# Optimization experiments

Hardware: AMD Instinct MI355X
Metric: run time of the kernel (lower is better)

The kernel has to match this reference:

```python
import jax, jax.numpy as jnp
import numpy as np

NEG_SLOPE = 0.2  # PyG GATConv default LeakyReLU slope
EPS = 1e-16


def gat_layer(x, W, a_src, a_dst, bias, src, dst, heads, out_dim, concat):
    N = x.shape[0]
    h = (x @ W).reshape(N, heads, out_dim)          # [N,H,C]
    alpha_src = (h * a_src).sum(-1)                  # [N,H]
    alpha_dst = (h * a_dst).sum(-1)                  # [N,H]
    e = jax.nn.leaky_relu(alpha_src[src] + alpha_dst[dst], NEG_SLOPE)  # [E,H]
    # segment softmax over incoming edges of each destination node
    m = jax.ops.segment_max(e, dst, num_segments=N)  # [N,H]
    p = jnp.exp(e - m[dst])
    denom = jax.ops.segment_sum(p, dst, num_segments=N)
    alpha = p / (denom[dst] + EPS)                   # [E,H]
    # scatter-aggregate messages to destinations
    out = jax.ops.segment_sum(alpha[:, :, None] * h[src], dst, num_segments=N)  # [N,H,C]
    out = out.reshape(N, heads * out_dim) if concat else out.mean(axis=1)
    return out + bias


def setup_inputs() -> dict:
    N, E, F_IN, NC = 100000, 1600000, 512, 10
    key = jax.random.key(0)
    ks = jax.random.split(key, 9)
    return {
        "x": jax.random.normal(ks[0], (N, F_IN), jnp.float32),
        "W1": jax.random.normal(ks[1], (F_IN, 64), jnp.float32) * (1.0 / np.sqrt(F_IN)),
        "att_src1": jax.random.normal(ks[2], (1, 8, 8), jnp.float32) * 0.1,
        "att_dst1": jax.random.normal(ks[3], (1, 8, 8), jnp.float32) * 0.1,
        "b1": jnp.zeros((64,), jnp.float32),
        "W2": jax.random.normal(ks[4], (64, NC), jnp.float32) * (1.0 / 8.0),
        "att_src2": jax.random.normal(ks[5], (1, 1, NC), jnp.float32) * 0.1,
        "att_dst2": jax.random.normal(ks[6], (1, 1, NC), jnp.float32) * 0.1,
        "b2": jnp.zeros((NC,), jnp.float32),
        "edge_index": jax.random.randint(ks[7], (2, E), 0, N, jnp.int64),
    }


def reference(x, W1, att_src1, att_dst1, b1, W2, att_src2, att_dst2, b2, edge_index):
    N = x.shape[0]
    # add self-loops (PyG GATConv add_self_loops=True default)
    loop = jnp.arange(N, dtype=edge_index.dtype)
    src = jnp.concatenate([edge_index[0], loop])
    dst = jnp.concatenate([edge_index[1], loop])
    h = gat_layer(x, W1, att_src1, att_dst1, b1, src, dst, heads=8, out_dim=8, concat=True)
    h = jax.nn.elu(h)
    nc = W2.shape[1]
    out = gat_layer(h, W2, att_src2, att_dst2, b2, src, dst, heads=1, out_dim=nc, concat=False)
    return jax.nn.log_softmax(out, axis=1)
```

## Files before the change

### kernel.cpp

```cpp
#include <hip/hip_runtime.h>
#include <math.h>

#define NEG 0.2f

typedef __bf16 bf16x4 __attribute__((ext_vector_type(4)));
typedef __bf16 bf16x8 __attribute__((ext_vector_type(8)));
typedef float  f32x4  __attribute__((ext_vector_type(4)));

__global__ __launch_bounds__(256) void gemm1_k(const float* __restrict__ x,
                                               const float* __restrict__ W1,
                                               float* __restrict__ h1, int Nn)
{
    __shared__ __bf16 xs[2][64][40];
    int t = threadIdx.x;
    int wave = t >> 6, lane = t & 63;
    int row0 = blockIdx.x * 64;
    int col0 = wave * 16;
    int lm = lane & 15;
    int lk = lane >> 4;

    bf16x8 bfrag[16];
#pragma unroll
    for (int ch = 0; ch < 16; ++ch) {
        int kb = ch * 32 + lk * 8;
#pragma unroll
        for (int j = 0; j < 8; ++j)
            bfrag[ch][j] = (__bf16)W1[(size_t)(kb + j) * 64 + col0 + lm];
    }

    f32x4 acc[4] = {};

    {
        int r = t >> 3, c4 = t & 7;
#pragma unroll
        for (int p = 0; p < 2; ++p) {
            int rr = p * 32 + r;
            int gr = row0 + rr;
            float4 v = make_float4(0.f, 0.f, 0.f, 0.f);
            if (gr < Nn) v = *(const float4*)(x + (size_t)gr * 512 + c4 * 4);
            bf16x4 b;
            b[0] = (__bf16)v.x; b[1] = (__bf16)v.y; b[2] = (__bf16)v.z; b[3] = (__bf16)v.w;
            *(bf16x4*)&xs[0][rr][c4 * 4] = b;
        }
    }
    __syncthreads();

#pragma unroll
    for (int ch = 0; ch < 16; ++ch) {
        int buf = ch & 1;
        if (ch < 15) {
            int kb = (ch + 1) * 32;
            int r = t >> 3, c4 = t & 7;
#pragma unroll
            for (int p = 0; p < 2; ++p) {
                int rr = p * 32 + r;
                int gr = row0 + rr;
                float4 v = make_float4(0.f, 0.f, 0.f, 0.f);
                if (gr < Nn) v = *(const float4*)(x + (size_t)gr * 512 + kb + c4 * 4);
                bf16x4 b;
                b[0] = (__bf16)v.x; b[1] = (__bf16)v.y; b[2] = (__bf16)v.z; b[3] = (__bf16)v.w;
                *(bf16x4*)&xs[1 - buf][rr][c4 * 4] = b;
            }
        }
#pragma unroll
        for (int rt = 0; rt < 4; ++rt) {
            bf16x8 a = *(bf16x8*)&xs[buf][rt * 16 + lm][lk * 8];
            acc[rt] = __builtin_amdgcn_mfma_f32_16x16x32_bf16(a, bfrag[ch], acc[rt], 0, 0, 0);
        }
        __syncthreads();
    }

#pragma unroll
    for (int rt = 0; rt < 4; ++rt) {
#pragma unroll
        for (int j = 0; j < 4; ++j) {
            int gr = row0 + rt * 16 + lk * 4 + j;
            if (gr < Nn) h1[(size_t)gr * 64 + col0 + lm] = acc[rt][j];
        }
    }
}

__global__ void attn1_k(const float* __restrict__ h1, const float* __restrict__ asrc,
                        const float* __restrict__ adst, float* __restrict__ as1,
                        float* __restrict__ ad1, int Nn)
{
    int tid = blockIdx.x * 256 + threadIdx.x;
    if (tid >= Nn * 8) return;
    int n = tid >> 3, h = tid & 7;
    const float* hp = h1 + (size_t)n * 64 + h * 8;
    float s = 0.f, d = 0.f;
#pragma unroll
    for (int c = 0; c < 8; ++c) {
        float v = hp[c];
        s += v * asrc[h * 8 + c];
        d += v * adst[h * 8 + c];
    }
    as1[tid] = s;
    ad1[tid] = d;
}

__global__ void hist_rank_k(const int* __restrict__ ei, int E, int Nn,
                            int* __restrict__ deg, int* __restrict__ rank)
{
    int e = blockIdx.x * 256 + threadIdx.x;
    int Ep = E + Nn;
    if (e >= Ep) return;
    int d = (e < E) ? ei[E + e] : e - E;
    rank[e] = atomicAdd(&deg[d], 1);
}

__global__ void scan_a_k(const int* __restrict__ deg, int Nn, int* __restrict__ bsum)
{
    __shared__ int tmp[256];
    int t = threadIdx.x;
    int base = blockIdx.x * 1024 + t * 4;
    int s = 0;
#pragma unroll
    for (int j = 0; j < 4; ++j) { int i = base + j; if (i < Nn) s += deg[i]; }
    tmp[t] = s;
    __syncthreads();
    for (int off = 1; off < 256; off <<= 1) {
        int a = (t >= off) ? tmp[t - off] : 0;
        __syncthreads();
        tmp[t] += a;
        __syncthreads();
    }
    if (t == 255) bsum[blockIdx.x] = tmp[255];
}

__global__ void scan_b_k(int* __restrict__ bsum, int nb)
{
    __shared__ int tmp[256];
    int t = threadIdx.x;
    int v = (t < nb) ? bsum[t] : 0;
    tmp[t] = v;
    __syncthreads();
    for (int off = 1; off < 256; off <<= 1) {
        int a = (t >= off) ? tmp[t - off] : 0;
        __syncthreads();
        tmp[t] += a;
        __syncthreads();
    }
    if (t < nb) bsum[t] = tmp[t] - v;
}

__global__ void scan_c_k(const int* __restrict__ deg, int Nn, const int* __restrict__ boff,
                         int* __restrict__ rowptr)
{
    __shared__ int tmp[256];
    int t = threadIdx.x;
    int base = blockIdx.x * 1024 + t * 4;
    int v[4];
    int s = 0;
#pragma unroll
    for (int j = 0; j < 4; ++j) {
        int i = base + j;
        v[j] = (i < Nn) ? deg[i] : 0;
        s += v[j];
    }
    tmp[t] = s;
    __syncthreads();
    for (int off = 1; off < 256; off <<= 1) {
        int a = (t >= off) ? tmp[t - off] : 0;
        __syncthreads();
        tmp[t] += a;
        __syncthreads();
    }
    int excl = boff[blockIdx.x] + tmp[t] - s;
#pragma unroll
    for (int j = 0; j < 4; ++j) {
        int i = base + j;
        if (i < Nn) {
            rowptr[i] = excl;
            excl += v[j];
            if (i == Nn - 1) rowptr[Nn] = excl;
        }
    }
}

__global__ void scat2_k(const int* __restrict__ ei, int E, int Nn,
                        const int* __restrict__ rowptr, const int* __restrict__ rank,
                        int* __restrict__ csr)
{
    int e = blockIdx.x * 256 + threadIdx.x;
    int Ep = E + Nn;
    if (e >= Ep) return;
    int s, d;
    if (e < E) { s = ei[e]; d = ei[E + e]; } else { s = d = e - E; }
    csr[rowptr[d] + rank[e]] = s;
}

__global__ __launch_bounds__(256) void agg1_k(const int* __restrict__ csr,
                                              const int* __restrict__ rowptr,
                                              const float* __restrict__ as1,
                                              const float* __restrict__ ad1,
                                              const float* __restrict__ h1,
                                              float* __restrict__ out1, int Nn)
{
    int wid = (blockIdx.x * 256 + threadIdx.x) >> 6;
    if (wid >= Nn) return;
    int lane = threadIdx.x & 63;
    int sub = lane >> 4;
    int c4 = lane & 15;
    int h = c4 >> 1;
    float adv = ad1[wid * 8 + h];
    int start = rowptr[wid];
    int len = rowptr[wid + 1] - start;
    float accp = 0.f;
    float4 accv = make_float4(0.f, 0.f, 0.f, 0.f);
    int i = sub;
    for (; i + 12 < len; i += 16) {
        int s0 = csr[start + i];
        int s1 = csr[start + i + 4];
        int s2 = csr[start + i + 8];
        int s3 = csr[start + i + 12];
        float e0 = as1[s0 * 8 + h] + adv;
        float e1 = as1[s1 * 8 + h] + adv;
        float e2 = as1[s2 * 8 + h] + adv;
        float e3 = as1[s3 * 8 + h] + adv;
        float4 hv0 = *(const float4*)(h1 + (size_t)s0 * 64 + c4 * 4);
        float4 hv1 = *(const float4*)(h1 + (size_t)s1 * 64 + c4 * 4);
        float4 hv2 = *(const float4*)(h1 + (size_t)s2 * 64 + c4 * 4);
        float4 hv3 = *(const float4*)(h1 + (size_t)s3 * 64 + c4 * 4);
        e0 = e0 > 0.f ? e0 : NEG * e0;
        e1 = e1 > 0.f ? e1 : NEG * e1;
        e2 = e2 > 0.f ? e2 : NEG * e2;
        e3 = e3 > 0.f ? e3 : NEG * e3;
        float p0 = __expf(e0), p1 = __expf(e1), p2 = __expf(e2), p3 = __expf(e3);
        accp += (p0 + p1) + (p2 + p3);
        accv.x += p0 * hv0.x + p1 * hv1.x + p2 * hv2.x + p3 * hv3.x;
        accv.y += p0 * hv0.y + p1 * hv1.y + p2 * hv2.y + p3 * hv3.y;
        accv.z += p0 * hv0.z + p1 * hv1.z + p2 * hv2.z + p3 * hv3.z;
        accv.w += p0 * hv0.w + p1 * hv1.w + p2 * hv2.w + p3 * hv3.w;
    }
    for (; i < len; i += 4) {
        int s0 = csr[start + i];
        float e0 = as1[s0 * 8 + h] + adv;
        float4 hv0 = *(const float4*)(h1 + (size_t)s0 * 64 + c4 * 4);
        e0 = e0 > 0.f ? e0 : NEG * e0;
        float p0 = __expf(e0);
        accp += p0;
        accv.x += p0 * hv0.x;
        accv.y += p0 * hv0.y;
        accv.z += p0 * hv0.z;
        accv.w += p0 * hv0.w;
    }
    accp   += __shfl_xor(accp, 16);
    accv.x += __shfl_xor(accv.x, 16);
    accv.y += __shfl_xor(accv.y, 16);
    accv.z += __shfl_xor(accv.z, 16);
    accv.w += __shfl_xor(accv.w, 16);
    accp   += __shfl_xor(accp, 32);
    accv.x += __shfl_xor(accv.x, 32);
    accv.y += __shfl_xor(accv.y, 32);
    accv.z += __shfl_xor(accv.z, 32);
    accv.w += __shfl_xor(accv.w, 32);
    if (sub == 0) {
        float inv = 1.f / (accp + 1e-16f);
        float4 o = make_float4(accv.x * inv, accv.y * inv, accv.z * inv, accv.w * inv);
        *(float4*)(out1 + (size_t)wid * 64 + c4 * 4) = o;
    }
}

__global__ void node2_k(const float* __restrict__ out1, const float* __restrict__ b1,
                        const float* __restrict__ W2, const float* __restrict__ as2w,
                        const float* __restrict__ ad2w, float* __restrict__ h2,
                        float* __restrict__ as2, float* __restrict__ ad2, int Nn)
{
    int n = blockIdx.x * 256 + threadIdx.x;
    if (n >= Nn) return;
    float g[64];
#pragma unroll
    for (int c = 0; c < 16; ++c) {
        float4 v = *(const float4*)(out1 + (size_t)n * 64 + c * 4);
        float4 b = *(const float4*)(b1 + c * 4);
        float t0 = v.x + b.x, t1 = v.y + b.y, t2 = v.z + b.z, t3 = v.w + b.w;
        g[c * 4 + 0] = t0 > 0.f ? t0 : expm1f(t0);
        g[c * 4 + 1] = t1 > 0.f ? t1 : expm1f(t1);
        g[c * 4 + 2] = t2 > 0.f ? t2 : expm1f(t2);
        g[c * 4 + 3] = t3 > 0.f ? t3 : expm1f(t3);
    }
    float acc[10] = {};
#pragma unroll
    for (int k = 0; k < 64; ++k) {
#pragma unroll
        for (int j = 0; j < 10; ++j) acc[j] += g[k] * W2[k * 10 + j];
    }
    float s = 0.f, d = 0.f;
#pragma unroll
    for (int j = 0; j < 10; ++j) {
        h2[(size_t)n * 16 + j] = acc[j];
        s += acc[j] * as2w[j];
        d += acc[j] * ad2w[j];
    }
    as2[n] = s;
    ad2[n] = d;
}

__global__ __launch_bounds__(256) void agg2_k(const int* __restrict__ csr,
                                              const int* __restrict__ rowptr,
                                              const float* __restrict__ as2,
                                              const float* __restrict__ ad2,
                                              const float* __restrict__ h2,
                                              float* __restrict__ out, int Nn)
{
    int wid = (blockIdx.x * 256 + threadIdx.x) >> 6;
    if (wid >= Nn) return;
    int lane = threadIdx.x & 63;
    int sub = lane >> 4;
    int c = lane & 15;
    float adv = ad2[wid];
    int start = rowptr[wid];
    int len = rowptr[wid + 1] - start;
    float accp = 0.f, accv = 0.f;
    int i = sub;
    for (; i + 12 < len; i += 16) {
        int s0 = csr[start + i];
        int s1 = csr[start + i + 4];
        int s2 = csr[start + i + 8];
        int s3 = csr[start + i + 12];
        float e0 = as2[s0] + adv;
        float e1 = as2[s1] + adv;
        float e2 = as2[s2] + adv;
        float e3 = as2[s3] + adv;
        float v0 = (c < 10) ? h2[(size_t)s0 * 16 + c] : 0.f;
        float v1 = (c < 10) ? h2[(size_t)s1 * 16 + c] : 0.f;
        float v2 = (c < 10) ? h2[(size_t)s2 * 16 + c] : 0.f;
        float v3 = (c < 10) ? h2[(size_t)s3 * 16 + c] : 0.f;
        e0 = e0 > 0.f ? e0 : NEG * e0;
        e1 = e1 > 0.f ? e1 : NEG * e1;
        e2 = e2 > 0.f ? e2 : NEG * e2;
        e3 = e3 > 0.f ? e3 : NEG * e3;
        float p0 = __expf(e0), p1 = __expf(e1), p2 = __expf(e2), p3 = __expf(e3);
        accp += (p0 + p1) + (p2 + p3);
        accv += p0 * v0 + p1 * v1 + p2 * v2 + p3 * v3;
    }
    for (; i < len; i += 4) {
        int s0 = csr[start + i];
        float e0 = as2[s0] + adv;
        float v0 = (c < 10) ? h2[(size_t)s0 * 16 + c] : 0.f;
        e0 = e0 > 0.f ? e0 : NEG * e0;
        float p0 = __expf(e0);
        accp += p0;
        accv += p0 * v0;
    }
    accp += __shfl_xor(accp, 16);
    accv += __shfl_xor(accv, 16);
    accp += __shfl_xor(accp, 32);
    accv += __shfl_xor(accv, 32);
    if (sub == 0 && c < 10)
        out[(size_t)wid * 10 + c] = accv / (accp + 1e-16f);
}

__global__ void lsm_k(float* __restrict__ out, const float* __restrict__ b2, int Nn)
{
    int n = blockIdx.x * 256 + threadIdx.x;
    if (n >= Nn) return;
    float z[10];
    float m = -1e30f;
#pragma unroll
    for (int j = 0; j < 10; ++j) {
        z[j] = out[(size_t)n * 10 + j] + b2[j];
        m = fmaxf(m, z[j]);
    }
    float ssum = 0.f;
#pragma unroll
    for (int j = 0; j < 10; ++j) ssum += expf(z[j] - m);
    float lse = m + logf(ssum);
#pragma unroll
    for (int j = 0; j < 10; ++j) out[(size_t)n * 10 + j] = z[j] - lse;
}

extern "C" void kernel_launch(void* const* d_in, const int* in_sizes, int n_in,
                              void* d_out, int out_size, void* d_ws, size_t ws_size,
                              hipStream_t stream)
{
    const float* x     = (const float*)d_in[0];
    const float* W1    = (const float*)d_in[1];
    const float* asrc1 = (const float*)d_in[2];
    const float* adst1 = (const float*)d_in[3];
    const float* b1    = (const float*)d_in[4];
    const float* W2    = (const float*)d_in[5];
    const float* asrc2 = (const float*)d_in[6];
    const float* adst2 = (const float*)d_in[7];
    const float* b2    = (const float*)d_in[8];
    const int*   ei    = (const int*)d_in[9];
    float* out = (float*)d_out;

    int F  = in_sizes[1] / 64;
    int Nn = in_sizes[0] / F;
    int E  = in_sizes[9] / 2;
    int Ep = E + Nn;
    int nb = (Nn + 1023) / 1024;

    float* f = (float*)d_ws;
    float* h1   = f;  f += (size_t)Nn * 64;
    float* as1  = f;  f += (size_t)Nn * 8;
    float* ad1  = f;  f += (size_t)Nn * 8;
    float* h2   = f;  f += (size_t)Nn * 16;
    float* as2  = f;  f += Nn;
    float* ad2  = f;  f += Nn;
    float* out1 = f;  f += (size_t)Nn * 64;
    int* ip = (int*)f;
    int* deg    = ip;  ip += Nn;
    int* rowptr = ip;  ip += Nn + 1;
    int* bsum   = ip;  ip += 256;
    int* rank   = ip;  ip += Ep;
    int* csr    = ip;  ip += Ep;

    hipMemsetAsync(deg, 0, (size_t)Nn * sizeof(int), stream);
    hist_rank_k<<<(Ep + 255) / 256, 256, 0, stream>>>(ei, E, Nn, deg, rank);
    scan_a_k<<<nb, 256, 0, stream>>>(deg, Nn, bsum);
    scan_b_k<<<1, 256, 0, stream>>>(bsum, nb);
    scan_c_k<<<nb, 256, 0, stream>>>(deg, Nn, bsum, rowptr);
    scat2_k<<<(Ep + 255) / 256, 256, 0, stream>>>(ei, E, Nn, rowptr, rank, csr);

    gemm1_k<<<(Nn + 63) / 64, 256, 0, stream>>>(x, W1, h1, Nn);
    attn1_k<<<(Nn * 8 + 255) / 256, 256, 0, stream>>>(h1, asrc1, adst1, as1, ad1, Nn);
    agg1_k<<<(Nn * 64 + 255) / 256, 256, 0, stream>>>(csr, rowptr, as1, ad1, h1, out1, Nn);

    node2_k<<<(Nn + 255) / 256, 256, 0, stream>>>(out1, b1, W2, asrc2, adst2, h2, as2, ad2, Nn);
    agg2_k<<<(Nn * 64 + 255) / 256, 256, 0, stream>>>(csr, rowptr, as2, ad2, h2, out, Nn);
    lsm_k<<<(Nn + 255) / 256, 256, 0, stream>>>(out, b2, Nn);
}
```

Baseline: 607.3 us.

## Pre-pack W1 to bf16 fragments and stream x directly into MFMA registers

```diff
diff --git a/kernel.cpp b/kernel.cpp
--- a/kernel.cpp
+++ b/kernel.cpp
@@ -3,79 +3,51 @@
 
 #define NEG 0.2f
 
-typedef __bf16 bf16x4 __attribute__((ext_vector_type(4)));
 typedef __bf16 bf16x8 __attribute__((ext_vector_type(8)));
 typedef float  f32x4  __attribute__((ext_vector_type(4)));
 
-__global__ __launch_bounds__(256) void gemm1_k(const float* __restrict__ x,
-                                               const float* __restrict__ W1,
-                                               float* __restrict__ h1, int Nn)
-{
-    __shared__ __bf16 xs[2][64][40];
+__global__ void w1prep_k(const float* __restrict__ W1, __bf16* __restrict__ W1b)
+{
+    int i = blockIdx.x * 256 + threadIdx.x;
+    int n = i & 63;
+    int k0 = (i >> 6) * 8;
+#pragma unroll
+    for (int j = 0; j < 8; ++j)
+        W1b[(size_t)i * 8 + j] = (__bf16)W1[(size_t)(k0 + j) * 64 + n];
+}
+
+__global__ __launch_bounds__(256, 4) void gemm1_k(const float* __restrict__ x,
+                                                  const __bf16* __restrict__ W1b,
+                                                  float* __restrict__ h1, int Nn)
+{
     int t = threadIdx.x;
     int wave = t >> 6, lane = t & 63;
-    int row0 = blockIdx.x * 64;
-    int col0 = wave * 16;
-    int lm = lane & 15;
-    int lk = lane >> 4;
-
-    bf16x8 bfrag[16];
+    int lm = lane & 15, lk = lane >> 4;
+    int rowa = blockIdx.x * 64 + wave * 16 + lm;
+    const float* xrow = x + (size_t)(rowa < Nn ? rowa : 0) * 512;
+    f32x4 acc[4] = {};
 #pragma unroll
     for (int ch = 0; ch < 16; ++ch) {
-        int kb = ch * 32 + lk * 8;
-#pragma unroll
-        for (int j = 0; j < 8; ++j)
-            bfrag[ch][j] = (__bf16)W1[(size_t)(kb + j) * 64 + col0 + lm];
-    }
-
-    f32x4 acc[4] = {};
-
-    {
-        int r = t >> 3, c4 = t & 7;
-#pragma unroll
-        for (int p = 0; p < 2; ++p) {
-            int rr = p * 32 + r;
-            int gr = row0 + rr;
-            float4 v = make_float4(0.f, 0.f, 0.f, 0.f);
-            if (gr < Nn) v = *(const float4*)(x + (size_t)gr * 512 + c4 * 4);
-            bf16x4 b;
-            b[0] = (__bf16)v.x; b[1] = (__bf16)v.y; b[2] = (__bf16)v.z; b[3] = (__bf16)v.w;
-            *(bf16x4*)&xs[0][rr][c4 * 4] = b;
+        float4 a0 = *(const float4*)(xrow + ch * 32 + lk * 8);
+        float4 a1 = *(const float4*)(xrow + ch * 32 + lk * 8 + 4);
+        bf16x8 af;
+        af[0] = (__bf16)a0.x; af[1] = (__bf16)a0.y;
+        af[2] = (__bf16)a0.z; af[3] = (__bf16)a0.w;
+        af[4] = (__bf16)a1.x; af[5] = (__bf16)a1.y;
+        af[6] = (__bf16)a1.z; af[7] = (__bf16)a1.w;
+#pragma unroll
+        for (int nt = 0; nt < 4; ++nt) {
+            bf16x8 bf = *(const bf16x8*)(W1b + ((size_t)((ch * 4 + lk) * 64) + nt * 16 + lm) * 8);
+            acc[nt] = __builtin_amdgcn_mfma_f32_16x16x32_bf16(af, bf, acc[nt], 0, 0, 0);
         }
     }
-    __syncthreads();
-
-#pragma unroll
-    for (int ch = 0; ch < 16; ++ch) {
-        int buf = ch & 1;
-        if (ch < 15) {
-            int kb = (ch + 1) * 32;
-            int r = t >> 3, c4 = t & 7;
-#pragma unroll
-            for (int p = 0; p < 2; ++p) {
-                int rr = p * 32 + r;
-                int gr = row0 + rr;
-                float4 v = make_float4(0.f, 0.f, 0.f, 0.f);
-                if (gr < Nn) v = *(const float4*)(x + (size_t)gr * 512 + kb + c4 * 4);
-                bf16x4 b;
-                b[0] = (__bf16)v.x; b[1] = (__bf16)v.y; b[2] = (__bf16)v.z; b[3] = (__bf16)v.w;
-                *(bf16x4*)&xs[1 - buf][rr][c4 * 4] = b;
-            }
-        }
-#pragma unroll
-        for (int rt = 0; rt < 4; ++rt) {
-            bf16x8 a = *(bf16x8*)&xs[buf][rt * 16 + lm][lk * 8];
-            acc[rt] = __builtin_amdgcn_mfma_f32_16x16x32_bf16(a, bfrag[ch], acc[rt], 0, 0, 0);
-        }
-        __syncthreads();
-    }
-
-#pragma unroll
-    for (int rt = 0; rt < 4; ++rt) {
+    int rowbase = blockIdx.x * 64 + wave * 16 + lk * 4;
+#pragma unroll
+    for (int nt = 0; nt < 4; ++nt) {
 #pragma unroll
         for (int j = 0; j < 4; ++j) {
-            int gr = row0 + rt * 16 + lk * 4 + j;
-            if (gr < Nn) h1[(size_t)gr * 64 + col0 + lm] = acc[rt][j];
+            int gr = rowbase + j;
+            if (gr < Nn) h1[(size_t)gr * 64 + nt * 16 + lm] = acc[nt][j];
         }
     }
 }
@@ -394,6 +366,7 @@
     int nb = (Nn + 1023) / 1024;
 
     float* f = (float*)d_ws;
+    __bf16* w1b = (__bf16*)f;  f += 512 * 64 / 2;
     float* h1   = f;  f += (size_t)Nn * 64;
     float* as1  = f;  f += (size_t)Nn * 8;
     float* ad1  = f;  f += (size_t)Nn * 8;
@@ -415,7 +388,8 @@
     scan_c_k<<<nb, 256, 0, stream>>>(deg, Nn, bsum, rowptr);
     scat2_k<<<(Ep + 255) / 256, 256, 0, stream>>>(ei, E, Nn, rowptr, rank, csr);
 
-    gemm1_k<<<(Nn + 63) / 64, 256, 0, stream>>>(x, W1, h1, Nn);
+    w1prep_k<<<16, 256, 0, stream>>>(W1, w1b);
+    gemm1_k<<<(Nn + 63) / 64, 256, 0, stream>>>(x, w1b, h1, Nn);
     attn1_k<<<(Nn * 8 + 255) / 256, 256, 0, stream>>>(h1, asrc1, adst1, as1, ad1, Nn);
     agg1_k<<<(Nn * 64 + 255) / 256, 256, 0, stream>>>(csr, rowptr, as1, ad1, h1, out1, Nn);
 
```

Measured after the change: 583.8 us. -3.9%, faster.
